# Optimization experiments

Measured on AMD Instinct MI355X. Metric: run time of the kernel, lower is better.

## Reference

```python
import jax, jax.numpy as jnp
import numpy as np

B, T, C, H = 4, 2048, 1024, 16
D = C // H


def setup_inputs() -> dict:
    key = jax.random.key(0)
    k1, k2, k3 = jax.random.split(key, 3)
    x = jax.random.normal(k1, (B, T, C), dtype=jnp.float32)
    attention_mask = jnp.zeros((B, 1, 1, T), dtype=jnp.float32)  # additive mask
    Wqkv = jax.random.normal(k2, (C, 3 * C), dtype=jnp.float32) * 0.02
    bqkv = jnp.zeros((3 * C,), dtype=jnp.float32)
    Wo = jax.random.normal(k3, (C, C), dtype=jnp.float32) * 0.02
    bo = jnp.zeros((C,), dtype=jnp.float32)
    return {"x": x, "attention_mask": attention_mask, "Wqkv": Wqkv,
            "bqkv": bqkv, "Wo": Wo, "bo": bo}


def reference(x, attention_mask, Wqkv, bqkv, Wo, bo):
    b, t, c = x.shape
    # Fused QKV projection
    qkv = x @ Wqkv + bqkv                      # [B, T, 3C]
    q, k, v = jnp.split(qkv, 3, axis=-1)       # each [B, T, C]
    # Split heads -> [B, H, T, D]
    def heads(z):
        return z.reshape(b, t, H, D).transpose(0, 2, 1, 3)
    q, k, v = heads(q), heads(k), heads(v)
    # Scaled dot-product attention, bidirectional, additive mask
    scale = 1.0 / jnp.sqrt(jnp.asarray(D, dtype=x.dtype))
    scores = jnp.einsum('bhtd,bhsd->bhts', q, k) * scale + attention_mask
    attn = jax.nn.softmax(scores, axis=-1)
    y = jnp.einsum('bhts,bhsd->bhtd', attn, v)  # [B, H, T, D]
    # Merge heads and output projection
    y = y.transpose(0, 2, 1, 3).reshape(b, t, c)
    return y @ Wo + bo
```

## Files before the change

### kernel.cpp

```cpp
#include <hip/hip_runtime.h>
#include <hip/hip_bf16.h>
#include <stdint.h>


typedef short s8v __attribute__((ext_vector_type(8)));
typedef float f4v __attribute__((ext_vector_type(4)));
typedef int   i2v __attribute__((ext_vector_type(2)));

#define MFMA16(a, b, c) __builtin_amdgcn_mfma_f32_16x16x32_bf16((a), (b), (c), 0, 0, 0)

__device__ __forceinline__ short f2bf(float f) {
  union { float f; unsigned u; } un; un.f = f;
  unsigned r = un.u + 0x7fffu + ((un.u >> 16) & 1u);
  return (short)(r >> 16);
}

__device__ __forceinline__ int cvtpk(float lo, float hi) {
  int r;
  asm("v_cvt_pk_bf16_f32 %0, %1, %2" : "=v"(r) : "v"(lo), "v"(hi));
  return r;
}

__device__ __forceinline__ void gll16(const void* g, void* l) {
  const __attribute__((address_space(1))) void* gp =
      (const __attribute__((address_space(1))) void*)(unsigned long long)(uintptr_t)g;
  __attribute__((address_space(3))) void* lp =
      (__attribute__((address_space(3))) void*)(unsigned int)(uintptr_t)l;
  __builtin_amdgcn_global_load_lds(gp, lp, 16, 0, 0);
}

__global__ __launch_bounds__(256)
void cast_bf16_k(const float* __restrict__ X, short* __restrict__ O, int n8) {
  int i = blockIdx.x * 256 + threadIdx.x;
  if (i >= n8) return;
  const f4v* xp = (const f4v*)X;
  f4v a = xp[2 * i], b = xp[2 * i + 1];
  s8v o;
  o[0] = f2bf(a[0]); o[1] = f2bf(a[1]); o[2] = f2bf(a[2]); o[3] = f2bf(a[3]);
  o[4] = f2bf(b[0]); o[5] = f2bf(b[1]); o[6] = f2bf(b[2]); o[7] = f2bf(b[3]);
  ((s8v*)O)[i] = o;
}

__global__ __launch_bounds__(256)
void transpose_cast(const float* __restrict__ W, short* __restrict__ WT, int R, int C0) {
  __shared__ float tile[32][33];
  const int t = threadIdx.x, tc = t & 31, tr = t >> 5;
  const int br = blockIdx.y * 32, bc = blockIdx.x * 32;
#pragma unroll
  for (int p = 0; p < 4; p++)
    tile[tr + p * 8][tc] = W[(size_t)(br + tr + p * 8) * C0 + bc + tc];
  __syncthreads();
#pragma unroll
  for (int p = 0; p < 4; p++)
    WT[(size_t)(bc + tr + p * 8) * R + br + tc] = f2bf(tile[tc][tr + p * 8]);
}

__global__ __launch_bounds__(256)
void transpose_v(const short* __restrict__ Vb, short* __restrict__ Vt) {
  __shared__ short tile[32][33];
  const int t = threadIdx.x, tc = t & 31, tr = t >> 5;
  const int bh = blockIdx.z;
  const int bt = blockIdx.x * 32, bd = blockIdx.y * 32;
  const short* src = Vb + (size_t)bh * 2048 * 64;
  short* dst = Vt + (size_t)bh * 64 * 2048;
#pragma unroll
  for (int p = 0; p < 4; p++)
    tile[tr + p * 8][tc] = src[(size_t)(bt + tr + p * 8) * 64 + bd + tc];
  __syncthreads();
#pragma unroll
  for (int p = 0; p < 4; p++)
    dst[(size_t)(bd + tr + p * 8) * 2048 + bt + tc] = tile[tc][tr + p * 8];
}

template <int EPI>
__global__ __launch_bounds__(256)
void gemm_bt(const short* __restrict__ A, const short* __restrict__ BT,
             const float* __restrict__ bias, float* __restrict__ outF,
             short* __restrict__ outQ, short* __restrict__ outK, short* __restrict__ outV,
             int K, int N) {
  __shared__ short As[128 * 32];
  __shared__ short Bs[128 * 32];
  const int t = threadIdx.x, w = t >> 6, l = t & 63, g = l >> 4, c = l & 15;
  const int wr = w >> 1, wc = w & 1;
  const int brow = blockIdx.y * 128, bcol = blockIdx.x * 128;

  const f4v z4 = {0.f, 0.f, 0.f, 0.f};
  f4v acc[4][4];
#pragma unroll
  for (int i = 0; i < 4; i++)
#pragma unroll
    for (int j = 0; j < 4; j++) acc[i][j] = z4;

  const int r0 = t >> 2, cb = (t & 3) * 8;
  const short* aS0 = A + (size_t)(brow + r0) * K + cb;
  const short* bS0 = BT + (size_t)(bcol + r0) * K + cb;
  char* AsB = (char*)As;
  char* BsB = (char*)Bs;

  for (int kt = 0; kt < K; kt += 32) {
    __syncthreads();
    gll16(aS0 + kt, AsB + w * 1024);
    gll16(aS0 + (size_t)64 * K + kt, AsB + 4096 + w * 1024);
    gll16(bS0 + kt, BsB + w * 1024);
    gll16(bS0 + (size_t)64 * K + kt, BsB + 4096 + w * 1024);
    asm volatile("s_waitcnt vmcnt(0)" ::: "memory");
    __syncthreads();

    s8v af[4], bf[4];
#pragma unroll
    for (int i = 0; i < 4; i++)
      af[i] = *(const s8v*)(As + (wr * 64 + i * 16 + c) * 32 + g * 8);
#pragma unroll
    for (int j = 0; j < 4; j++)
      bf[j] = *(const s8v*)(Bs + (wc * 64 + j * 16 + c) * 32 + g * 8);
#pragma unroll
    for (int i = 0; i < 4; i++)
#pragma unroll
      for (int j = 0; j < 4; j++) acc[i][j] = MFMA16(af[i], bf[j], acc[i][j]);
  }

#pragma unroll
  for (int i = 0; i < 4; i++) {
    const int mB = brow + wr * 64 + i * 16 + g * 4;
#pragma unroll
    for (int j = 0; j < 4; j++) {
      const int n = bcol + wc * 64 + j * 16 + c;
      const float bv = bias[n];
#pragma unroll
      for (int r = 0; r < 4; r++) {
        float v = acc[i][j][r] + bv;
        const int mm = mB + r;
        if (EPI == 1) {
          outF[(size_t)mm * N + n] = v;
        } else {
          const int b = mm >> 11, tt = mm & 2047;
          const int seg = n >> 10, nn = n & 1023;
          const int h = nn >> 6, d = nn & 63;
          const size_t idx = (((size_t)b * 16 + h) * 2048 + tt) * 64 + d;
          if (seg == 0)      outQ[idx] = f2bf(v * 0.18033688f);
          else if (seg == 1) outK[idx] = f2bf(v);
          else               outV[idx] = f2bf(v);
        }
      }
    }
  }
}

__global__ __launch_bounds__(256, 4)
void flash_attn(const short* __restrict__ Q, const short* __restrict__ Kg,
                const short* __restrict__ Vt, const float* __restrict__ mask,
                short* __restrict__ Y) {
  __shared__ short Kl[64][72];
  __shared__ short Vl[64][72];
  __shared__ short Pl[4][16][72];
  const int t = threadIdx.x, w = t >> 6, l = t & 63, g = l >> 4, c = l & 15;
  const int bh = blockIdx.x, b = bh >> 4, h = bh & 15;
  const int qbase = blockIdx.y * 64 + w * 16;

  const short* Qp = Q + (size_t)bh * 2048 * 64;
  const short* Kp = Kg + (size_t)bh * 2048 * 64;
  const short* Vp = Vt + (size_t)bh * 64 * 2048;
  const float* mrowp = mask + (size_t)b * 2048;

  s8v qf0, qf1;
  {
    const short* qsrc = Qp + (size_t)(qbase + c) * 64 + g * 8;
    qf0 = *(const s8v*)qsrc;
    qf1 = *(const s8v*)(qsrc + 32);
  }

  const f4v z4 = {0.f, 0.f, 0.f, 0.f};
  f4v po[4];
#pragma unroll
  for (int d4 = 0; d4 < 4; d4++) po[d4] = z4;
  float mrun = -3e38f;
  float lrun = 0.f;

  const int rr = t >> 3, cbs = (t & 7) * 8;
  const short* ks0 = Kp + (size_t)rr * 64 + cbs;
  const short* vs0 = Vp + (size_t)rr * 2048 + cbs;

  s8v k0r = *(const s8v*)(ks0);
  s8v k1r = *(const s8v*)(ks0 + 32 * 64);
  s8v v0r = *(const s8v*)(vs0);
  s8v v1r = *(const s8v*)(vs0 + (size_t)32 * 2048);

  const float L2E = 1.44269504f;

  for (int kt = 0; kt < 32; ++kt) {
    __syncthreads();
    *(s8v*)(&Kl[rr][cbs]) = k0r;
    *(s8v*)(&Kl[rr + 32][cbs]) = k1r;
    *(s8v*)(&Vl[rr][cbs]) = v0r;
    *(s8v*)(&Vl[rr + 32][cbs]) = v1r;
    __syncthreads();
    if (kt < 31) {
      k0r = *(const s8v*)(ks0 + (size_t)(kt + 1) * 4096);
      k1r = *(const s8v*)(ks0 + (size_t)(kt + 1) * 4096 + 32 * 64);
      v0r = *(const s8v*)(vs0 + (kt + 1) * 64);
      v1r = *(const s8v*)(vs0 + (kt + 1) * 64 + (size_t)32 * 2048);
    }

    f4v mk[4];
#pragma unroll
    for (int j = 0; j < 4; j++)
      mk[j] = *(const f4v*)(mrowp + kt * 64 + j * 16 + g * 4);

    f4v sv[4];
#pragma unroll
    for (int j = 0; j < 4; j++) sv[j] = z4;
#pragma unroll
    for (int j = 0; j < 4; j++) {
      s8v kf0 = *(const s8v*)(&Kl[j * 16 + c][g * 8]);
      s8v kf1 = *(const s8v*)(&Kl[j * 16 + c][32 + g * 8]);
      sv[j] = MFMA16(kf0, qf0, sv[j]);
      sv[j] = MFMA16(kf1, qf1, sv[j]);
    }

    s8v vf0[4], vf1[4];
#pragma unroll
    for (int d4 = 0; d4 < 4; d4++) {
      vf0[d4] = *(const s8v*)(&Vl[d4 * 16 + c][g * 8]);
      vf1[d4] = *(const s8v*)(&Vl[d4 * 16 + c][32 + g * 8]);
    }

    float sp[4][4];
#pragma unroll
    for (int j = 0; j < 4; j++)
#pragma unroll
      for (int r = 0; r < 4; r++) sp[j][r] = fmaf(mk[j][r], L2E, sv[j][r]);

    float pm = fmaxf(fmaxf(fmaxf(sp[0][0], sp[0][1]), fmaxf(sp[0][2], sp[0][3])),
                     fmaxf(fmaxf(sp[1][0], sp[1][1]), fmaxf(sp[1][2], sp[1][3])));
    pm = fmaxf(pm, fmaxf(fmaxf(fmaxf(sp[2][0], sp[2][1]), fmaxf(sp[2][2], sp[2][3])),
                         fmaxf(fmaxf(sp[3][0], sp[3][1]), fmaxf(sp[3][2], sp[3][3]))));
    pm = fmaxf(pm, __shfl_xor(pm, 16));
    pm = fmaxf(pm, __shfl_xor(pm, 32));

    if (__any(pm > mrun + 7.0f)) {
      const float mn = fmaxf(mrun, pm);
      const float al = exp2f(mrun - mn);
      lrun *= al;
      mrun = mn;
      const int ali = __float_as_int(al);
      const float aq0 = __int_as_float(__builtin_amdgcn_ds_bpermute(g * 16, ali));
      const float aq1 = __int_as_float(__builtin_amdgcn_ds_bpermute(g * 16 + 4, ali));
      const float aq2 = __int_as_float(__builtin_amdgcn_ds_bpermute(g * 16 + 8, ali));
      const float aq3 = __int_as_float(__builtin_amdgcn_ds_bpermute(g * 16 + 12, ali));
#pragma unroll
      for (int d4 = 0; d4 < 4; d4++) {
        f4v o = po[d4];
        o[0] *= aq0; o[1] *= aq1; o[2] *= aq2; o[3] *= aq3;
        po[d4] = o;
      }
    }

    float ps = 0.f;
    int wlo[4], whi[4];
#pragma unroll
    for (int j = 0; j < 4; j++) {
      const float p0 = exp2f(sp[j][0] - mrun);
      const float p1 = exp2f(sp[j][1] - mrun);
      const float p2 = exp2f(sp[j][2] - mrun);
      const float p3 = exp2f(sp[j][3] - mrun);
      ps += (p0 + p1) + (p2 + p3);
      wlo[j] = cvtpk(p0, p1);
      whi[j] = cvtpk(p2, p3);
    }
    ps += __shfl_xor(ps, 16);
    ps += __shfl_xor(ps, 32);
    lrun += ps;

#pragma unroll
    for (int j = 0; j < 4; j++) {
      i2v wv; wv[0] = wlo[j]; wv[1] = whi[j];
      *(i2v*)(&Pl[w][c][j * 16 + g * 4]) = wv;
    }
    s8v pa0 = *(const s8v*)(&Pl[w][c][g * 8]);
    s8v pa1 = *(const s8v*)(&Pl[w][c][32 + g * 8]);

#pragma unroll
    for (int d4 = 0; d4 < 4; d4++) {
      po[d4] = MFMA16(pa0, vf0[d4], po[d4]);
      po[d4] = MFMA16(pa1, vf1[d4], po[d4]);
    }
  }

  {
    const int li = __float_as_int(lrun);
    float linv[4];
#pragma unroll
    for (int r = 0; r < 4; r++)
      linv[r] = 1.0f / __int_as_float(__builtin_amdgcn_ds_bpermute(g * 16 + r * 4, li));
#pragma unroll
    for (int d4 = 0; d4 < 4; d4++) {
#pragma unroll
      for (int r = 0; r < 4; r++) {
        const float ov = po[d4][r] * linv[r];
        const int tt = qbase + g * 4 + r;
        const int dd = d4 * 16 + c;
        Y[((size_t)b * 2048 + tt) * 1024 + h * 64 + dd] = f2bf(ov);
      }
    }
  }
}

extern "C" void kernel_launch(void* const* d_in, const int* in_sizes, int n_in,
                              void* d_out, int out_size, void* d_ws, size_t ws_size,
                              hipStream_t stream) {
  (void)in_sizes; (void)n_in; (void)out_size; (void)ws_size;
  const float* x    = (const float*)d_in[0];
  const float* mask = (const float*)d_in[1];
  const float* Wqkv = (const float*)d_in[2];
  const float* bqkv = (const float*)d_in[3];
  const float* Wo   = (const float*)d_in[4];
  const float* bo   = (const float*)d_in[5];
  float* out = (float*)d_out;

  char* ws = (char*)d_ws;
  const size_t M16 = 16777216;
  short* xb  = (short*)(ws);
  short* Vt  = (short*)(ws);
  short* Wqt = (short*)(ws + M16);
  short* Wot = (short*)(ws + M16 + 6291456);
  short* Qb  = (short*)(ws + 25165824);
  short* Kb  = (short*)(ws + 25165824 + M16);
  short* Vb  = (short*)(ws + 25165824 + 2 * M16);
  short* Yb  = Vb;

  cast_bf16_k<<<4096, 256, 0, stream>>>(x, xb, 1048576);
  transpose_cast<<<dim3(96, 32), 256, 0, stream>>>(Wqkv, Wqt, 1024, 3072);
  transpose_cast<<<dim3(32, 32), 256, 0, stream>>>(Wo, Wot, 1024, 1024);
  gemm_bt<0><<<dim3(24, 64), 256, 0, stream>>>(xb, Wqt, bqkv, nullptr, Qb, Kb, Vb, 1024, 3072);
  transpose_v<<<dim3(64, 2, 64), 256, 0, stream>>>(Vb, Vt);
  flash_attn<<<dim3(64, 32), 256, 0, stream>>>(Qb, Kb, Vt, mask, Yb);
  gemm_bt<1><<<dim3(8, 64), 256, 0, stream>>>(Yb, Wot, bo, out, nullptr, nullptr, nullptr, 1024, 1024);
}
```

Measured before the change: 363.9 us.

## Rework attention to 32x32 MFMA with mask folded into V and row-sum MFMA

The flash attention kernel moves from 16x16x32 to 32x32x16 MFMA tiles, so each wave handles 32 query rows and builds the P operand in registers with permlane32 swaps instead of round-tripping through LDS. The additive mask is turned into a multiplicative weight exp(mask), which is folded into V during the transpose and also used in an extra MFMA that accumulates the softmax denominator. This removes the per-tile mask loads and the shuffle reductions of the row sum. In exchange it uses more registers, with launch bounds lowered to 2 blocks per SM, and a bf16 exp(mask) weight can overflow or lose precision for large or -inf masks.

```diff
diff --git a/kernel.cpp b/kernel.cpp
--- a/kernel.cpp
+++ b/kernel.cpp
@@ -3,24 +3,31 @@
 #include <stdint.h>
 
 
-typedef short s8v __attribute__((ext_vector_type(8)));
-typedef float f4v __attribute__((ext_vector_type(4)));
-typedef int   i2v __attribute__((ext_vector_type(2)));
+typedef short s8v  __attribute__((ext_vector_type(8)));
+typedef float f4v  __attribute__((ext_vector_type(4)));
+typedef float f16v __attribute__((ext_vector_type(16)));
+typedef int   i4v  __attribute__((ext_vector_type(4)));
 
 #define MFMA16(a, b, c) __builtin_amdgcn_mfma_f32_16x16x32_bf16((a), (b), (c), 0, 0, 0)
+#define MFMA32(a, b, c) __builtin_amdgcn_mfma_f32_32x32x16_bf16((a), (b), (c), 0, 0, 0)
 
 __device__ __forceinline__ short f2bf(float f) {
   union { float f; unsigned u; } un; un.f = f;
   unsigned r = un.u + 0x7fffu + ((un.u >> 16) & 1u);
   return (short)(r >> 16);
 }
-
+__device__ __forceinline__ float bf2f(short s) {
+  union { unsigned u; float f; } un; un.u = ((unsigned)(unsigned short)s) << 16;
+  return un.f;
+}
 __device__ __forceinline__ int cvtpk(float lo, float hi) {
   int r;
   asm("v_cvt_pk_bf16_f32 %0, %1, %2" : "=v"(r) : "v"(lo), "v"(hi));
   return r;
 }
-
+__device__ __forceinline__ void plswap(int& d, int& s) {
+  asm volatile("v_permlane32_swap_b32 %0, %1" : "+v"(d), "+v"(s));
+}
 __device__ __forceinline__ void gll16(const void* g, void* l) {
   const __attribute__((address_space(1))) void* gp =
       (const __attribute__((address_space(1))) void*)(unsigned long long)(uintptr_t)g;
@@ -42,6 +49,12 @@
 }
 
 __global__ __launch_bounds__(256)
+void mask2w(const float* __restrict__ mask, short* __restrict__ wb, int n) {
+  int i = blockIdx.x * 256 + threadIdx.x;
+  if (i < n) wb[i] = f2bf(exp2f(mask[i] * 1.44269504f));
+}
+
+__global__ __launch_bounds__(256)
 void transpose_cast(const float* __restrict__ W, short* __restrict__ WT, int R, int C0) {
   __shared__ float tile[32][33];
   const int t = threadIdx.x, tc = t & 31, tr = t >> 5;
@@ -56,20 +69,23 @@
 }
 
 __global__ __launch_bounds__(256)
-void transpose_v(const short* __restrict__ Vb, short* __restrict__ Vt) {
-  __shared__ short tile[32][33];
+void transpose_v(const short* __restrict__ Vb, const short* __restrict__ wb,
+                 short* __restrict__ Vt) {
+  __shared__ float tile[32][33];
   const int t = threadIdx.x, tc = t & 31, tr = t >> 5;
-  const int bh = blockIdx.z;
+  const int bh = blockIdx.z, b = bh >> 4;
   const int bt = blockIdx.x * 32, bd = blockIdx.y * 32;
   const short* src = Vb + (size_t)bh * 2048 * 64;
   short* dst = Vt + (size_t)bh * 64 * 2048;
 #pragma unroll
+  for (int p = 0; p < 4; p++) {
+    const int trow = bt + tr + p * 8;
+    tile[tr + p * 8][tc] = bf2f(src[(size_t)trow * 64 + bd + tc]) * bf2f(wb[b * 2048 + trow]);
+  }
+  __syncthreads();
+#pragma unroll
   for (int p = 0; p < 4; p++)
-    tile[tr + p * 8][tc] = src[(size_t)(bt + tr + p * 8) * 64 + bd + tc];
-  __syncthreads();
-#pragma unroll
-  for (int p = 0; p < 4; p++)
-    dst[(size_t)(bd + tr + p * 8) * 2048 + bt + tc] = tile[tc][tr + p * 8];
+    dst[(size_t)(bd + tr + p * 8) * 2048 + bt + tc] = f2bf(tile[tc][tr + p * 8]);
 }
 
 template <int EPI>
@@ -146,53 +162,46 @@
   }
 }
 
-__global__ __launch_bounds__(256, 4)
+__global__ __launch_bounds__(256, 2)
 void flash_attn(const short* __restrict__ Q, const short* __restrict__ Kg,
-                const short* __restrict__ Vt, const float* __restrict__ mask,
+                const short* __restrict__ Vt, const short* __restrict__ wb,
                 short* __restrict__ Y) {
   __shared__ short Kl[64][72];
   __shared__ short Vl[64][72];
-  __shared__ short Pl[4][16][72];
-  const int t = threadIdx.x, w = t >> 6, l = t & 63, g = l >> 4, c = l & 15;
+  const int t = threadIdx.x, w = t >> 6, L = t & 63, hi = L >> 5, c = L & 31;
   const int bh = blockIdx.x, b = bh >> 4, h = bh & 15;
-  const int qbase = blockIdx.y * 64 + w * 16;
+  const int qrow = blockIdx.y * 128 + w * 32;
 
   const short* Qp = Q + (size_t)bh * 2048 * 64;
   const short* Kp = Kg + (size_t)bh * 2048 * 64;
   const short* Vp = Vt + (size_t)bh * 64 * 2048;
-  const float* mrowp = mask + (size_t)b * 2048;
-
-  s8v qf0, qf1;
-  {
-    const short* qsrc = Qp + (size_t)(qbase + c) * 64 + g * 8;
-    qf0 = *(const s8v*)qsrc;
-    qf1 = *(const s8v*)(qsrc + 32);
-  }
-
-  const f4v z4 = {0.f, 0.f, 0.f, 0.f};
-  f4v po[4];
-#pragma unroll
-  for (int d4 = 0; d4 < 4; d4++) po[d4] = z4;
-  float mrun = -3e38f;
-  float lrun = 0.f;
-
-  const int rr = t >> 3, cbs = (t & 7) * 8;
-  const short* ks0 = Kp + (size_t)rr * 64 + cbs;
-  const short* vs0 = Vp + (size_t)rr * 2048 + cbs;
+  const short* wp = wb + b * 2048;
+
+  s8v qf[4];
+#pragma unroll
+  for (int s = 0; s < 4; s++)
+    qf[s] = *(const s8v*)(Qp + (size_t)(qrow + c) * 64 + s * 16 + hi * 8);
+
+  f16v po0, po1, ls;
+#pragma unroll
+  for (int r = 0; r < 16; r++) { po0[r] = 0.f; po1[r] = 0.f; ls[r] = 0.f; }
+  float mrun = 0.f;
+
+  const int rr = t >> 3, ch = (t & 7) * 8;
+  const short* ks0 = Kp + (size_t)rr * 64 + ch;
+  const short* vs0 = Vp + (size_t)rr * 2048 + ch;
 
   s8v k0r = *(const s8v*)(ks0);
   s8v k1r = *(const s8v*)(ks0 + 32 * 64);
   s8v v0r = *(const s8v*)(vs0);
   s8v v1r = *(const s8v*)(vs0 + (size_t)32 * 2048);
 
-  const float L2E = 1.44269504f;
-
   for (int kt = 0; kt < 32; ++kt) {
     __syncthreads();
-    *(s8v*)(&Kl[rr][cbs]) = k0r;
-    *(s8v*)(&Kl[rr + 32][cbs]) = k1r;
-    *(s8v*)(&Vl[rr][cbs]) = v0r;
-    *(s8v*)(&Vl[rr + 32][cbs]) = v1r;
+    *(s8v*)(&Kl[rr][ch]) = k0r;
+    *(s8v*)(&Kl[rr + 32][ch]) = k1r;
+    *(s8v*)(&Vl[rr][ch]) = v0r;
+    *(s8v*)(&Vl[rr + 32][ch]) = v1r;
     __syncthreads();
     if (kt < 31) {
       k0r = *(const s8v*)(ks0 + (size_t)(kt + 1) * 4096);
@@ -201,107 +210,94 @@
       v1r = *(const s8v*)(vs0 + (kt + 1) * 64 + (size_t)32 * 2048);
     }
 
-    f4v mk[4];
-#pragma unroll
-    for (int j = 0; j < 4; j++)
-      mk[j] = *(const f4v*)(mrowp + kt * 64 + j * 16 + g * 4);
-
-    f4v sv[4];
-#pragma unroll
-    for (int j = 0; j < 4; j++) sv[j] = z4;
-#pragma unroll
-    for (int j = 0; j < 4; j++) {
-      s8v kf0 = *(const s8v*)(&Kl[j * 16 + c][g * 8]);
-      s8v kf1 = *(const s8v*)(&Kl[j * 16 + c][32 + g * 8]);
-      sv[j] = MFMA16(kf0, qf0, sv[j]);
-      sv[j] = MFMA16(kf1, qf1, sv[j]);
-    }
-
-    s8v vf0[4], vf1[4];
-#pragma unroll
-    for (int d4 = 0; d4 < 4; d4++) {
-      vf0[d4] = *(const s8v*)(&Vl[d4 * 16 + c][g * 8]);
-      vf1[d4] = *(const s8v*)(&Vl[d4 * 16 + c][32 + g * 8]);
-    }
-
-    float sp[4][4];
-#pragma unroll
-    for (int j = 0; j < 4; j++)
-#pragma unroll
-      for (int r = 0; r < 4; r++) sp[j][r] = fmaf(mk[j][r], L2E, sv[j][r]);
-
-    float pm = fmaxf(fmaxf(fmaxf(sp[0][0], sp[0][1]), fmaxf(sp[0][2], sp[0][3])),
-                     fmaxf(fmaxf(sp[1][0], sp[1][1]), fmaxf(sp[1][2], sp[1][3])));
-    pm = fmaxf(pm, fmaxf(fmaxf(fmaxf(sp[2][0], sp[2][1]), fmaxf(sp[2][2], sp[2][3])),
-                         fmaxf(fmaxf(sp[3][0], sp[3][1]), fmaxf(sp[3][2], sp[3][3]))));
-    pm = fmaxf(pm, __shfl_xor(pm, 16));
+    s8v wf[4];
+#pragma unroll
+    for (int s2 = 0; s2 < 4; s2++)
+      wf[s2] = *(const s8v*)(wp + kt * 64 + s2 * 16 + hi * 8);
+
+    f16v s0, s1;
+#pragma unroll
+    for (int r = 0; r < 16; r++) { s0[r] = 0.f; s1[r] = 0.f; }
+#pragma unroll
+    for (int s = 0; s < 4; s++) {
+      s8v ka0 = *(const s8v*)(&Kl[c][s * 16 + hi * 8]);
+      s8v ka1 = *(const s8v*)(&Kl[32 + c][s * 16 + hi * 8]);
+      s0 = MFMA32(ka0, qf[s], s0);
+      s1 = MFMA32(ka1, qf[s], s1);
+    }
+
+    float pm = s0[0];
+#pragma unroll
+    for (int r = 1; r < 16; r++) pm = fmaxf(pm, s0[r]);
+#pragma unroll
+    for (int r = 0; r < 16; r++) pm = fmaxf(pm, s1[r]);
     pm = fmaxf(pm, __shfl_xor(pm, 32));
 
-    if (__any(pm > mrun + 7.0f)) {
+    if (kt == 0) {
+      mrun = pm;
+    } else if (__any(pm > mrun + 7.0f)) {
       const float mn = fmaxf(mrun, pm);
       const float al = exp2f(mrun - mn);
-      lrun *= al;
       mrun = mn;
       const int ali = __float_as_int(al);
-      const float aq0 = __int_as_float(__builtin_amdgcn_ds_bpermute(g * 16, ali));
-      const float aq1 = __int_as_float(__builtin_amdgcn_ds_bpermute(g * 16 + 4, ali));
-      const float aq2 = __int_as_float(__builtin_amdgcn_ds_bpermute(g * 16 + 8, ali));
-      const float aq3 = __int_as_float(__builtin_amdgcn_ds_bpermute(g * 16 + 12, ali));
-#pragma unroll
-      for (int d4 = 0; d4 < 4; d4++) {
-        f4v o = po[d4];
-        o[0] *= aq0; o[1] *= aq1; o[2] *= aq2; o[3] *= aq3;
-        po[d4] = o;
+#pragma unroll
+      for (int r = 0; r < 16; r++) {
+        const int qm = (r & 3) + 8 * (r >> 2) + 4 * hi;
+        const float alr = __int_as_float(__builtin_amdgcn_ds_bpermute(qm * 4, ali));
+        ls[r] *= alr; po0[r] *= alr; po1[r] *= alr;
       }
     }
 
-    float ps = 0.f;
-    int wlo[4], whi[4];
-#pragma unroll
-    for (int j = 0; j < 4; j++) {
-      const float p0 = exp2f(sp[j][0] - mrun);
-      const float p1 = exp2f(sp[j][1] - mrun);
-      const float p2 = exp2f(sp[j][2] - mrun);
-      const float p3 = exp2f(sp[j][3] - mrun);
-      ps += (p0 + p1) + (p2 + p3);
-      wlo[j] = cvtpk(p0, p1);
-      whi[j] = cvtpk(p2, p3);
-    }
-    ps += __shfl_xor(ps, 16);
-    ps += __shfl_xor(ps, 32);
-    lrun += ps;
-
-#pragma unroll
-    for (int j = 0; j < 4; j++) {
-      i2v wv; wv[0] = wlo[j]; wv[1] = whi[j];
-      *(i2v*)(&Pl[w][c][j * 16 + g * 4]) = wv;
-    }
-    s8v pa0 = *(const s8v*)(&Pl[w][c][g * 8]);
-    s8v pa1 = *(const s8v*)(&Pl[w][c][32 + g * 8]);
-
-#pragma unroll
-    for (int d4 = 0; d4 < 4; d4++) {
-      po[d4] = MFMA16(pa0, vf0[d4], po[d4]);
-      po[d4] = MFMA16(pa1, vf1[d4], po[d4]);
-    }
-  }
-
-  {
-    const int li = __float_as_int(lrun);
-    float linv[4];
-#pragma unroll
-    for (int r = 0; r < 4; r++)
-      linv[r] = 1.0f / __int_as_float(__builtin_amdgcn_ds_bpermute(g * 16 + r * 4, li));
-#pragma unroll
-    for (int d4 = 0; d4 < 4; d4++) {
-#pragma unroll
-      for (int r = 0; r < 4; r++) {
-        const float ov = po[d4][r] * linv[r];
-        const int tt = qbase + g * 4 + r;
-        const int dd = d4 * 16 + c;
-        Y[((size_t)b * 2048 + tt) * 1024 + h * 64 + dd] = f2bf(ov);
+    f16v p0, p1;
+#pragma unroll
+    for (int r = 0; r < 16; r++) {
+      p0[r] = exp2f(s0[r] - mrun);
+      p1[r] = exp2f(s1[r] - mrun);
+    }
+
+    s8v pa[4];
+#pragma unroll
+    for (int s2 = 0; s2 < 4; s2++) {
+      const int sg = (s2 & 1) * 8;
+      int w0, w1, w2, w3;
+      {
+        int e0 = (s2 < 2) ? cvtpk(p0[sg + 0], p0[sg + 1]) : cvtpk(p1[sg + 0], p1[sg + 1]);
+        int e1 = (s2 < 2) ? cvtpk(p0[sg + 4], p0[sg + 5]) : cvtpk(p1[sg + 4], p1[sg + 5]);
+        plswap(e0, e1);
+        w0 = e0; w2 = e1;
       }
-    }
+      {
+        int e0 = (s2 < 2) ? cvtpk(p0[sg + 2], p0[sg + 3]) : cvtpk(p1[sg + 2], p1[sg + 3]);
+        int e1 = (s2 < 2) ? cvtpk(p0[sg + 6], p0[sg + 7]) : cvtpk(p1[sg + 6], p1[sg + 7]);
+        plswap(e0, e1);
+        w1 = e0; w3 = e1;
+      }
+      union { i4v i; s8v s; } u;
+      u.i[0] = w0; u.i[1] = w1; u.i[2] = w2; u.i[3] = w3;
+      pa[s2] = u.s;
+    }
+
+#pragma unroll
+    for (int s2 = 0; s2 < 4; s2++) ls = MFMA32(pa[s2], wf[s2], ls);
+#pragma unroll
+    for (int s2 = 0; s2 < 4; s2++) {
+      s8v vb0 = *(const s8v*)(&Vl[c][s2 * 16 + hi * 8]);
+      po0 = MFMA32(pa[s2], vb0, po0);
+    }
+#pragma unroll
+    for (int s2 = 0; s2 < 4; s2++) {
+      s8v vb1 = *(const s8v*)(&Vl[32 + c][s2 * 16 + hi * 8]);
+      po1 = MFMA32(pa[s2], vb1, po1);
+    }
+  }
+
+#pragma unroll
+  for (int r = 0; r < 16; r++) {
+    const float li = __builtin_amdgcn_rcpf(ls[r]);
+    const int qm = (r & 3) + 8 * (r >> 2) + 4 * hi;
+    const size_t base = ((size_t)b * 2048 + qrow + qm) * 1024 + h * 64;
+    Y[base + c] = f2bf(po0[r] * li);
+    Y[base + 32 + c] = f2bf(po1[r] * li);
   }
 }
 
@@ -322,6 +318,7 @@
   short* xb  = (short*)(ws);
   short* Vt  = (short*)(ws);
   short* Wqt = (short*)(ws + M16);
+  short* wbp = Wqt;
   short* Wot = (short*)(ws + M16 + 6291456);
   short* Qb  = (short*)(ws + 25165824);
   short* Kb  = (short*)(ws + 25165824 + M16);
@@ -332,7 +329,8 @@
   transpose_cast<<<dim3(96, 32), 256, 0, stream>>>(Wqkv, Wqt, 1024, 3072);
   transpose_cast<<<dim3(32, 32), 256, 0, stream>>>(Wo, Wot, 1024, 1024);
   gemm_bt<0><<<dim3(24, 64), 256, 0, stream>>>(xb, Wqt, bqkv, nullptr, Qb, Kb, Vb, 1024, 3072);
-  transpose_v<<<dim3(64, 2, 64), 256, 0, stream>>>(Vb, Vt);
-  flash_attn<<<dim3(64, 32), 256, 0, stream>>>(Qb, Kb, Vt, mask, Yb);
+  mask2w<<<32, 256, 0, stream>>>(mask, wbp, 8192);
+  transpose_v<<<dim3(64, 2, 64), 256, 0, stream>>>(Vb, wbp, Vt);
+  flash_attn<<<dim3(64, 16), 256, 0, stream>>>(Qb, Kb, Vt, wbp, Yb);
   gemm_bt<1><<<dim3(8, 64), 256, 0, stream>>>(Yb, Wot, bo, out, nullptr, nullptr, nullptr, 1024, 1024);
 }
```

New measurement: 333.9 us. -8.2%, faster.
